# Kernel optimization log

Hardware: AMD Instinct MI355X
Metric: run time of the kernel (lower is better)

## Reference

```python
import jax, jax.numpy as jnp
import numpy as np
from jax import lax

B, L, C, H, W = 4, 64, 64, 32, 32
K = 3
CONN = 4


def _conv(x, w, b):
    # x: (N, C_in, H, W), w: (C_out, C_in, K, K) -- stride 1, pad K//2 (same as nn.Conv2d)
    p = K // 2
    y = lax.conv_general_dilated(x, w, window_strides=(1, 1), padding=[(p, p), (p, p)],
                                 dimension_numbers=("NCHW", "OIHW", "NCHW"))
    return y + b[None, :, None, None]


def _neighbours_sum(n, m):
    # n: (B*L, C, H, W); m: (B, L, L) bool adjacency with CONN True per row.
    # Equivalent to masked_select + view(B,L,CONN,C,H,W).sum(2): a masked neighbor sum.
    nb = n.reshape(B, L, C, H, W)
    o = jnp.einsum("bij,bjchw->bichw", m.astype(n.dtype), nb)
    return o.reshape(B * L, C, H, W)


def setup_inputs() -> dict:
    key = jax.random.key(0)
    ks = jax.random.split(key, 9)
    fan0 = 1.0 / np.sqrt(C * K * K)
    x = jax.random.normal(ks[0], (B * L, C, H, W), dtype=jnp.float32)
    w_x0 = jax.random.uniform(ks[1], (C, C, K, K), jnp.float32, -fan0, fan0)
    b_x0 = jax.random.uniform(ks[2], (C,), jnp.float32, -fan0, fan0)
    w_n0 = jax.random.uniform(ks[3], (C, C, K, K), jnp.float32, -fan0, fan0)
    b_n0 = jax.random.uniform(ks[4], (C,), jnp.float32, -fan0, fan0)
    w_x1 = jax.random.uniform(ks[5], (C, C, K, K), jnp.float32, -fan0, fan0)
    b_x1 = jax.random.uniform(ks[6], (C,), jnp.float32, -fan0, fan0)
    w_n1 = jax.random.uniform(ks[7], (C, C, K, K), jnp.float32, -fan0, fan0)
    b_n1 = jax.random.uniform(ks[8], (C,), jnp.float32, -fan0, fan0)
    # adjacency with exactly CONN neighbors per (b, i) row
    rng = np.random.default_rng(0)
    idx = np.argsort(rng.random((B, L, L)), axis=-1)[..., :CONN]
    mask = np.zeros((B, L, L), dtype=bool)
    np.put_along_axis(mask, idx, True, axis=-1)
    return {"x": x, "w_x0": w_x0, "b_x0": b_x0, "w_n0": w_n0, "b_n0": b_n0,
            "w_x1": w_x1, "b_x1": b_x1, "w_n1": w_n1, "b_n1": b_n1,
            "neighbours_matrix": jnp.asarray(mask), "connected_num": 4}


def reference(x, w_x0, b_x0, w_n0, b_n0, w_x1, b_x1, w_n1, b_n1, neighbours_matrix, connected_num):
    residual = x
    n_set = _conv(x, w_n0, b_n0)
    h = _conv(x, w_x0, b_x0)
    h = jax.nn.relu(h + _neighbours_sum(n_set, neighbours_matrix))
    n_set = _conv(h, w_n1, b_n1)
    h2 = _conv(h, w_x1, b_x1)
    h2 = h2 + _neighbours_sum(n_set, neighbours_matrix)
    return jax.nn.relu(h2 + residual)
```

## Files before the change

### kernel.cpp

```cpp
#include <hip/hip_runtime.h>

#define NIMG 256
#define CCH 64
#define HWSZ 1024
#define IMG_NHWC 65536

typedef __attribute__((ext_vector_type(8))) short  s16x8;
typedef __attribute__((ext_vector_type(4))) short  s16x4;
typedef __attribute__((ext_vector_type(4))) float  f32x4;

__device__ __forceinline__ unsigned short f2bf(float f) {
    unsigned u = __builtin_bit_cast(unsigned, f);
    u += 0x7fffu + ((u >> 16) & 1u);
    return (unsigned short)(u >> 16);
}
__device__ __forceinline__ float bf2f(unsigned short h) {
    unsigned u = ((unsigned)h) << 16;
    return __builtin_bit_cast(float, u);
}

__device__ __forceinline__ void gload_lds16(const void* g, void* l) {
    __builtin_amdgcn_global_load_lds(
        (const __attribute__((address_space(1))) unsigned int*)g,
        (__attribute__((address_space(3))) unsigned int*)l, 16, 0, 0);
}

__global__ __launch_bounds__(256) void build_nbr_kernel(const unsigned char* __restrict__ mraw,
                                                        int* __restrict__ nbr) {
    __shared__ int nz;
    int t = threadIdx.x;
    if (t == 0) nz = 0;
    __syncthreads();
    int local = 0;
    for (int i = t; i < 16384; i += 256) local += (mraw[i] != 0) ? 1 : 0;
    atomicAdd(&nz, local);
    __syncthreads();
    bool isByte = (nz == 1024);
    const int* mi = (const int*)mraw;
    int c = 0;
    int base = t * 64;
    for (int j = 0; j < 64; ++j) {
        int v = isByte ? (int)mraw[base + j] : mi[base + j];
        if (v != 0 && c < 4) { nbr[t * 4 + c] = j; ++c; }
    }
    for (; c < 4; ++c) nbr[t * 4 + c] = -1;
}

__global__ __launch_bounds__(256) void pack_w_kernel(const float* __restrict__ w0,
                                                     const float* __restrict__ w1,
                                                     const float* __restrict__ w2,
                                                     const float* __restrict__ w3,
                                                     unsigned short* __restrict__ wp) {
    int idx = blockIdx.x * 256 + threadIdx.x;
    if (idx >= 147456) return;
    int e  = idx & 7;
    int sp = (idx >> 3) & 7;
    int co = (idx >> 6) & 63;
    int tc = idx >> 12;
    int cv = tc / 9, tap = tc - cv * 9;
    int ci = ((sp ^ (co & 7)) << 3) + e;
    const float* w = (cv == 0) ? w0 : (cv == 1) ? w1 : (cv == 2) ? w2 : w3;
    wp[idx] = f2bf(w[(co * 64 + ci) * 9 + tap]);
}

__global__ __launch_bounds__(256) void to_nhwc_kernel(const float* __restrict__ x,
                                                      unsigned short* __restrict__ xb) {
    __shared__ unsigned short lds[256 * 68];
    int bid = blockIdx.x;
    int n = bid >> 2, px0 = (bid & 3) * 256;
    int t = threadIdx.x, w = t >> 6, l = t & 63;

    #pragma unroll
    for (int pp = 0; pp < 8; ++pp) {
        int c = w * 16 + pp * 2;
        const float* s0 = x + ((size_t)(n * 64 + c)) * HWSZ + px0;
        const float* s1 = s0 + HWSZ;
        #pragma unroll
        for (int ch = 0; ch < 4; ++ch) {
            int px = ch * 64 + l;
            unsigned pack = (unsigned)f2bf(s0[px]) | ((unsigned)f2bf(s1[px]) << 16);
            *(unsigned*)((char*)lds + px * 136 + c * 2) = pack;
        }
    }
    __syncthreads();
    #pragma unroll
    for (int it = 0; it < 8; ++it) {
        int pos = it * 256 + t;
        int px = pos >> 3, c0 = (pos & 7) * 8;
        const char* src = (const char*)lds + px * 136 + c0 * 2;
        s16x4 v0 = *(const s16x4*)src;
        s16x4 v1 = *(const s16x4*)(src + 8);
        unsigned short* dst = xb + ((size_t)(n * 1024) + px0 + px) * 64 + c0;
        *(s16x4*)dst = v0;
        *(s16x4*)(dst + 4) = v1;
    }
}

__global__ __launch_bounds__(256, 2) void conv_mfma_kernel(const unsigned short* __restrict__ act,
                                                           const unsigned short* __restrict__ wconv,
                                                           const float* __restrict__ bias,
                                                           unsigned short* __restrict__ outp) {
    __shared__ unsigned short lds[10 * 34 * 64];
    __shared__ unsigned short wbuf[2][4096];
    int bid = blockIdx.x;
    int n = bid >> 2, stripe = bid & 3;
    int y0 = stripe * 8;
    int t = threadIdx.x, w = t >> 6, l = t & 63;

    {
        const unsigned short* img = act + ((size_t)n << 16);
        int x1 = (t >> 3) & 31, slot = t & 7;
        int c = x1 + 1;
        int sslot = slot ^ (c & 7);
        char* ldsbase = (char*)lds + (w * 8 + 1) * 128;
        #pragma unroll
        for (int r = 0; r < 10; ++r) {
            int y = y0 - 1 + r;
            if (y >= 0 && y < 32) {
                gload_lds16(img + (y * 32 + x1) * 64 + sslot * 8, ldsbase + r * 4352);
            } else {
                s16x8 z = {0,0,0,0,0,0,0,0};
                *(s16x8*)((char*)lds + r * 4352 + c * 128 + slot * 16) = z;
            }
        }
        if (t < 160) {
            int r = t >> 4, cp = ((t >> 3) & 1) ? 33 : 0, sl = t & 7;
            s16x8 z = {0,0,0,0,0,0,0,0};
            int off = ((r * 34 + cp) * 128 + sl * 16) ^ ((cp & 7) << 4);
            *(s16x8*)((char*)lds + off) = z;
        }
        #pragma unroll
        for (int j = 0; j < 2; ++j) {
            int chunk = (j * 4 + w) * 1024;
            gload_lds16((const char*)wconv + chunk + l * 16,
                        (char*)&wbuf[0][0] + chunk);
        }
    }
    __syncthreads();

    int lm = l & 15, kg = l >> 4;
    f32x4 acc[4][4];
    #pragma unroll
    for (int m = 0; m < 4; ++m)
        #pragma unroll
        for (int p = 0; p < 4; ++p) acc[m][p] = (f32x4){0.f, 0.f, 0.f, 0.f};

    #pragma unroll
    for (int tap = 0; tap < 9; ++tap) {
        if (tap < 8) {
            const char* wsb = (const char*)wconv + (tap + 1) * 8192;
            char* wdb = (char*)&wbuf[(tap + 1) & 1][0];
            #pragma unroll
            for (int j = 0; j < 2; ++j) {
                int chunk = (j * 4 + w) * 1024;
                gload_lds16(wsb + chunk + l * 16, wdb + chunk);
            }
        }
        const int dy = tap / 3, dx = tap % 3;
        const char* wb = (const char*)&wbuf[tap & 1][0];
        #pragma unroll
        for (int g = 0; g < 2; ++g) {
            s16x8 a[4], bfr[4];
            #pragma unroll
            for (int m = 0; m < 4; ++m) {
                int row = m * 16 + lm;
                int ao  = row * 128 + (((g * 4 + kg) ^ (lm & 7)) * 16);
                a[m] = *(const s16x8*)(wb + ao);
            }
            #pragma unroll
            for (int p = 0; p < 4; ++p) {
                int r  = 2 * w + (p >> 1) + dy;
                int xl = (p & 1) * 16 + lm + dx;
                int lb = (r * 4352 + xl * 128 + g * 64 + kg * 16) ^ ((xl & 7) << 4);
                bfr[p] = *(const s16x8*)((const char*)lds + lb);
            }
            #pragma unroll
            for (int m = 0; m < 4; ++m)
                #pragma unroll
                for (int p = 0; p < 4; ++p)
                    acc[m][p] = __builtin_amdgcn_mfma_f32_16x16x32_bf16(a[m], bfr[p], acc[m][p], 0, 0, 0);
        }
        if (tap < 8) __syncthreads();
    }

    #pragma unroll
    for (int m = 0; m < 4; ++m) {
        f32x4 bv = *(const f32x4*)(bias + m * 16 + kg * 4);
        #pragma unroll
        for (int p = 0; p < 4; ++p) {
            int y  = y0 + 2 * w + (p >> 1);
            int xx = (p & 1) * 16 + lm;
            s16x4 o;
            #pragma unroll
            for (int j = 0; j < 4; ++j) o[j] = (short)f2bf(acc[m][p][j] + bv[j]);
            *(s16x4*)(outp + (((size_t)n * 1024 + y * 32 + xx) * 64) + m * 16 + kg * 4) = o;
        }
    }
}

__global__ __launch_bounds__(256) void agg_relu_kernel(unsigned short* __restrict__ hx,
                                                       const unsigned short* __restrict__ nset,
                                                       const int* __restrict__ nbr) {
    int bid = blockIdx.x;
    int n = bid >> 5;
    int b = n >> 6;
    int rem = ((bid & 31) << 8) + threadIdx.x;
    size_t u = (((size_t)n) << 13) + rem;
    s16x8 hv = *(const s16x8*)(hx + u * 8);
    float s[8];
    #pragma unroll
    for (int j = 0; j < 8; ++j) s[j] = bf2f((unsigned short)hv[j]);
    #pragma unroll
    for (int k = 0; k < 4; ++k) {
        int jn = nbr[n * 4 + k];
        if (jn >= 0) {
            s16x8 nv = *(const s16x8*)(nset + ((((size_t)(b * 64 + jn)) << 13) + rem) * 8);
            #pragma unroll
            for (int j = 0; j < 8; ++j) s[j] += bf2f((unsigned short)nv[j]);
        }
    }
    s16x8 o;
    #pragma unroll
    for (int j = 0; j < 8; ++j) o[j] = (short)f2bf(fmaxf(s[j], 0.f));
    *(s16x8*)(hx + u * 8) = o;
}

__global__ __launch_bounds__(256) void final_kernel(const unsigned short* __restrict__ h2x,
                                                    const unsigned short* __restrict__ nset,
                                                    const int* __restrict__ nbr,
                                                    const float* __restrict__ x,
                                                    float* __restrict__ out) {
    __shared__ float lds[128 * 68];
    int bid = blockIdx.x;
    int n = bid >> 3, px0 = (bid & 7) * 128;
    int b = n >> 6;
    int t = threadIdx.x;
    int j0 = nbr[n * 4 + 0], j1 = nbr[n * 4 + 1], j2 = nbr[n * 4 + 2], j3 = nbr[n * 4 + 3];
    size_t base = ((size_t)n * 1024 + px0) * 64;
    size_t nb[4];
    nb[0] = ((size_t)(b * 64 + (j0 < 0 ? 0 : j0)) * 1024 + px0) * 64;
    nb[1] = ((size_t)(b * 64 + (j1 < 0 ? 0 : j1)) * 1024 + px0) * 64;
    nb[2] = ((size_t)(b * 64 + (j2 < 0 ? 0 : j2)) * 1024 + px0) * 64;
    nb[3] = ((size_t)(b * 64 + (j3 < 0 ? 0 : j3)) * 1024 + px0) * 64;
    int use[4] = {j0 >= 0, j1 >= 0, j2 >= 0, j3 >= 0};

    #pragma unroll
    for (int it = 0; it < 4; ++it) {
        int pos = it * 256 + t;
        int px = pos >> 3, c0 = (pos & 7) * 8;
        int off = px * 64 + c0;
        float s[8];
        s16x8 hv = *(const s16x8*)(h2x + base + off);
        #pragma unroll
        for (int j = 0; j < 8; ++j) s[j] = bf2f((unsigned short)hv[j]);
        #pragma unroll
        for (int k = 0; k < 4; ++k) {
            if (use[k]) {
                s16x8 nv = *(const s16x8*)(nset + nb[k] + off);
                #pragma unroll
                for (int j = 0; j < 8; ++j) s[j] += bf2f((unsigned short)nv[j]);
            }
        }
        float* dst = &lds[px * 68 + c0];
        *(f32x4*)dst = (f32x4){s[0], s[1], s[2], s[3]};
        *(f32x4*)(dst + 4) = (f32x4){s[4], s[5], s[6], s[7]};
    }
    __syncthreads();

    int w = t >> 6, l = t & 63;
    #pragma unroll
    for (int q = 0; q < 4; ++q) {
        int c0 = w * 16 + q * 4;
        #pragma unroll
        for (int half = 0; half < 2; ++half) {
            int px = half * 64 + l;
            f32x4 v = *(const f32x4*)&lds[px * 68 + c0];
            #pragma unroll
            for (int j = 0; j < 4; ++j) {
                size_t a = ((size_t)(n * 64) + c0 + j) * HWSZ + px0 + px;
                out[a] = fmaxf(v[j] + x[a], 0.f);
            }
        }
    }
}

extern "C" void kernel_launch(void* const* d_in, const int* in_sizes, int n_in,
                              void* d_out, int out_size, void* d_ws, size_t ws_size,
                              hipStream_t stream) {
    const float* x    = (const float*)d_in[0];
    const float* w_x0 = (const float*)d_in[1];
    const float* b_x0 = (const float*)d_in[2];
    const float* w_n0 = (const float*)d_in[3];
    const float* b_n0 = (const float*)d_in[4];
    const float* w_x1 = (const float*)d_in[5];
    const float* b_x1 = (const float*)d_in[6];
    const float* w_n1 = (const float*)d_in[7];
    const float* b_n1 = (const float*)d_in[8];
    const unsigned char* mask = (const unsigned char*)d_in[9];

    unsigned short* xb    = (unsigned short*)d_ws;
    unsigned short* hxb   = xb  + (size_t)NIMG * IMG_NHWC;
    unsigned short* nsetb = hxb + (size_t)NIMG * IMG_NHWC;
    unsigned short* wpack = nsetb + (size_t)NIMG * IMG_NHWC;
    int* nbr = (int*)(wpack + 147456);

    build_nbr_kernel<<<1, 256, 0, stream>>>(mask, nbr);
    pack_w_kernel<<<576, 256, 0, stream>>>(w_n0, w_x0, w_n1, w_x1, wpack);
    to_nhwc_kernel<<<1024, 256, 0, stream>>>(x, xb);

    const unsigned short* wp_n0 = wpack;
    const unsigned short* wp_x0 = wpack + 36864;
    const unsigned short* wp_n1 = wpack + 73728;
    const unsigned short* wp_x1 = wpack + 110592;

    conv_mfma_kernel<<<1024, 256, 0, stream>>>(xb, wp_n0, b_n0, nsetb);
    conv_mfma_kernel<<<1024, 256, 0, stream>>>(xb, wp_x0, b_x0, hxb);
    agg_relu_kernel<<<8192, 256, 0, stream>>>(hxb, nsetb, nbr);

    conv_mfma_kernel<<<1024, 256, 0, stream>>>(hxb, wp_n1, b_n1, nsetb);
    conv_mfma_kernel<<<1024, 256, 0, stream>>>(hxb, wp_x1, b_x1, xb);
    final_kernel<<<2048, 256, 0, stream>>>(xb, nsetb, nbr, x, (float*)d_out);
}
```

Before: 325.5 us.

## Make conv blocks per-image with resident weights and double-buffered input stripes

Each conv block now processes a whole image: all nine weight taps are loaded into LDS once and reused across four row stripes. The next stripe's input tile is prefetched into a second buffer while the current one is computed. This removes repeated weight loads and per-tap barriers, at the cost of large LDS use, one block per CU, and a quarter as many blocks.

```diff
diff --git a/kernel.cpp b/kernel.cpp
--- a/kernel.cpp
+++ b/kernel.cpp
@@ -96,105 +96,115 @@
     }
 }
 
-__global__ __launch_bounds__(256, 2) void conv_mfma_kernel(const unsigned short* __restrict__ act,
+__global__ __launch_bounds__(256, 1) void conv_mfma_kernel(const unsigned short* __restrict__ act,
                                                            const unsigned short* __restrict__ wconv,
                                                            const float* __restrict__ bias,
                                                            unsigned short* __restrict__ outp) {
-    __shared__ unsigned short lds[10 * 34 * 64];
-    __shared__ unsigned short wbuf[2][4096];
-    int bid = blockIdx.x;
-    int n = bid >> 2, stripe = bid & 3;
-    int y0 = stripe * 8;
+    __shared__ unsigned short wlds[36864];
+    __shared__ unsigned short inb[2][10 * 34 * 64];
+    int n = blockIdx.x;
     int t = threadIdx.x, w = t >> 6, l = t & 63;
 
+    const unsigned short* img = act + ((size_t)n << 16);
+    int x1 = (t >> 3) & 31, slot = t & 7;
+    int c = x1 + 1;
+    int sslot = slot ^ (c & 7);
+
+    #pragma unroll
+    for (int j = 0; j < 18; ++j) {
+        int off = j * 4096 + w * 1024;
+        gload_lds16((const char*)wconv + off + l * 16, (char*)wlds + off);
+    }
     {
-        const unsigned short* img = act + ((size_t)n << 16);
-        int x1 = (t >> 3) & 31, slot = t & 7;
-        int c = x1 + 1;
-        int sslot = slot ^ (c & 7);
-        char* ldsbase = (char*)lds + (w * 8 + 1) * 128;
+        char* ldsbase = (char*)inb[0] + (w * 8 + 1) * 128;
         #pragma unroll
         for (int r = 0; r < 10; ++r) {
-            int y = y0 - 1 + r;
-            if (y >= 0 && y < 32) {
+            int y = -1 + r;
+            if (y >= 0) {
                 gload_lds16(img + (y * 32 + x1) * 64 + sslot * 8, ldsbase + r * 4352);
             } else {
                 s16x8 z = {0,0,0,0,0,0,0,0};
-                *(s16x8*)((char*)lds + r * 4352 + c * 128 + slot * 16) = z;
+                *(s16x8*)((char*)inb[0] + r * 4352 + c * 128 + slot * 16) = z;
             }
         }
         if (t < 160) {
             int r = t >> 4, cp = ((t >> 3) & 1) ? 33 : 0, sl = t & 7;
             s16x8 z = {0,0,0,0,0,0,0,0};
             int off = ((r * 34 + cp) * 128 + sl * 16) ^ ((cp & 7) << 4);
-            *(s16x8*)((char*)lds + off) = z;
-        }
-        #pragma unroll
-        for (int j = 0; j < 2; ++j) {
-            int chunk = (j * 4 + w) * 1024;
-            gload_lds16((const char*)wconv + chunk + l * 16,
-                        (char*)&wbuf[0][0] + chunk);
+            *(s16x8*)((char*)inb[0] + off) = z;
+            *(s16x8*)((char*)inb[1] + off) = z;
         }
     }
     __syncthreads();
 
     int lm = l & 15, kg = l >> 4;
-    f32x4 acc[4][4];
-    #pragma unroll
-    for (int m = 0; m < 4; ++m)
-        #pragma unroll
-        for (int p = 0; p < 4; ++p) acc[m][p] = (f32x4){0.f, 0.f, 0.f, 0.f};
-
-    #pragma unroll
-    for (int tap = 0; tap < 9; ++tap) {
-        if (tap < 8) {
-            const char* wsb = (const char*)wconv + (tap + 1) * 8192;
-            char* wdb = (char*)&wbuf[(tap + 1) & 1][0];
-            #pragma unroll
-            for (int j = 0; j < 2; ++j) {
-                int chunk = (j * 4 + w) * 1024;
-                gload_lds16(wsb + chunk + l * 16, wdb + chunk);
-            }
-        }
-        const int dy = tap / 3, dx = tap % 3;
-        const char* wb = (const char*)&wbuf[tap & 1][0];
-        #pragma unroll
-        for (int g = 0; g < 2; ++g) {
-            s16x8 a[4], bfr[4];
-            #pragma unroll
-            for (int m = 0; m < 4; ++m) {
-                int row = m * 16 + lm;
-                int ao  = row * 128 + (((g * 4 + kg) ^ (lm & 7)) * 16);
-                a[m] = *(const s16x8*)(wb + ao);
-            }
+
+    #pragma unroll
+    for (int s = 0; s < 4; ++s) {
+        if (s < 3) {
+            int y0n = (s + 1) * 8;
+            char* ldsbase = (char*)inb[(s + 1) & 1] + (w * 8 + 1) * 128;
+            #pragma unroll
+            for (int r = 0; r < 10; ++r) {
+                int y = y0n - 1 + r;
+                if (y < 32) {
+                    gload_lds16(img + (y * 32 + x1) * 64 + sslot * 8, ldsbase + r * 4352);
+                } else {
+                    s16x8 z = {0,0,0,0,0,0,0,0};
+                    *(s16x8*)((char*)inb[(s + 1) & 1] + r * 4352 + c * 128 + slot * 16) = z;
+                }
+            }
+        }
+
+        const char* tile = (const char*)inb[s & 1];
+        f32x4 acc[4][4];
+        #pragma unroll
+        for (int m = 0; m < 4; ++m)
+            #pragma unroll
+            for (int p = 0; p < 4; ++p) acc[m][p] = (f32x4){0.f, 0.f, 0.f, 0.f};
+
+        #pragma unroll
+        for (int tap = 0; tap < 9; ++tap) {
+            const int dy = tap / 3, dx = tap % 3;
+            #pragma unroll
+            for (int g = 0; g < 2; ++g) {
+                s16x8 a[4], bfr[4];
+                #pragma unroll
+                for (int m = 0; m < 4; ++m) {
+                    int row = m * 16 + lm;
+                    int ao  = tap * 8192 + row * 128 + (((g * 4 + kg) ^ (lm & 7)) * 16);
+                    a[m] = *(const s16x8*)((const char*)wlds + ao);
+                }
+                #pragma unroll
+                for (int p = 0; p < 4; ++p) {
+                    int r  = 2 * w + (p >> 1) + dy;
+                    int xl = (p & 1) * 16 + lm + dx;
+                    int lb = (r * 4352 + xl * 128 + g * 64 + kg * 16) ^ ((xl & 7) << 4);
+                    bfr[p] = *(const s16x8*)(tile + lb);
+                }
+                #pragma unroll
+                for (int m = 0; m < 4; ++m)
+                    #pragma unroll
+                    for (int p = 0; p < 4; ++p)
+                        acc[m][p] = __builtin_amdgcn_mfma_f32_16x16x32_bf16(a[m], bfr[p], acc[m][p], 0, 0, 0);
+            }
+        }
+
+        int y0 = s * 8;
+        #pragma unroll
+        for (int m = 0; m < 4; ++m) {
+            f32x4 bv = *(const f32x4*)(bias + m * 16 + kg * 4);
             #pragma unroll
             for (int p = 0; p < 4; ++p) {
-                int r  = 2 * w + (p >> 1) + dy;
-                int xl = (p & 1) * 16 + lm + dx;
-                int lb = (r * 4352 + xl * 128 + g * 64 + kg * 16) ^ ((xl & 7) << 4);
-                bfr[p] = *(const s16x8*)((const char*)lds + lb);
-            }
-            #pragma unroll
-            for (int m = 0; m < 4; ++m)
-                #pragma unroll
-                for (int p = 0; p < 4; ++p)
-                    acc[m][p] = __builtin_amdgcn_mfma_f32_16x16x32_bf16(a[m], bfr[p], acc[m][p], 0, 0, 0);
-        }
-        if (tap < 8) __syncthreads();
-    }
-
-    #pragma unroll
-    for (int m = 0; m < 4; ++m) {
-        f32x4 bv = *(const f32x4*)(bias + m * 16 + kg * 4);
-        #pragma unroll
-        for (int p = 0; p < 4; ++p) {
-            int y  = y0 + 2 * w + (p >> 1);
-            int xx = (p & 1) * 16 + lm;
-            s16x4 o;
-            #pragma unroll
-            for (int j = 0; j < 4; ++j) o[j] = (short)f2bf(acc[m][p][j] + bv[j]);
-            *(s16x4*)(outp + (((size_t)n * 1024 + y * 32 + xx) * 64) + m * 16 + kg * 4) = o;
-        }
+                int y  = y0 + 2 * w + (p >> 1);
+                int xx = (p & 1) * 16 + lm;
+                s16x4 o;
+                #pragma unroll
+                for (int j = 0; j < 4; ++j) o[j] = (short)f2bf(acc[m][p][j] + bv[j]);
+                *(s16x4*)(outp + (((size_t)n * 1024 + y * 32 + xx) * 64) + m * 16 + kg * 4) = o;
+            }
+        }
+        if (s < 3) __syncthreads();
     }
 }
 
@@ -313,11 +323,11 @@
     const unsigned short* wp_n1 = wpack + 73728;
     const unsigned short* wp_x1 = wpack + 110592;
 
-    conv_mfma_kernel<<<1024, 256, 0, stream>>>(xb, wp_n0, b_n0, nsetb);
-    conv_mfma_kernel<<<1024, 256, 0, stream>>>(xb, wp_x0, b_x0, hxb);
+    conv_mfma_kernel<<<256, 256, 0, stream>>>(xb, wp_n0, b_n0, nsetb);
+    conv_mfma_kernel<<<256, 256, 0, stream>>>(xb, wp_x0, b_x0, hxb);
     agg_relu_kernel<<<8192, 256, 0, stream>>>(hxb, nsetb, nbr);
 
-    conv_mfma_kernel<<<1024, 256, 0, stream>>>(hxb, wp_n1, b_n1, nsetb);
-    conv_mfma_kernel<<<1024, 256, 0, stream>>>(hxb, wp_x1, b_x1, xb);
+    conv_mfma_kernel<<<256, 256, 0, stream>>>(hxb, wp_n1, b_n1, nsetb);
+    conv_mfma_kernel<<<256, 256, 0, stream>>>(hxb, wp_x1, b_x1, xb);
     final_kernel<<<2048, 256, 0, stream>>>(xb, nsetb, nbr, x, (float*)d_out);
 }
```

New measurement: 318.8 us. 2.1% less time.
